# Kernel tuning notes

Measured on AMD Instinct MI355X. Metric: run time of the kernel, lower is better.

Reference implementation:

```python
import jax, jax.numpy as jnp
import numpy as np

NODE_TYPE_SIZE = 9      # common.NodeType.SIZE in MeshGraphNets
N_NODES = 1_000_000
N_CELLS = 2_000_000


def setup_inputs() -> dict:
    key = jax.random.key(0)
    k1, k2, k3, k4, k5 = jax.random.split(key, 5)
    world_pos = jax.random.normal(k1, (1, N_NODES, 3), dtype=jnp.float32)
    prev_world_pos = world_pos + 0.01 * jax.random.normal(k2, (1, N_NODES, 3), dtype=jnp.float32)
    mesh_pos = jax.random.normal(k3, (1, N_NODES, 3), dtype=jnp.float32)
    node_type = jax.random.randint(k4, (1, N_NODES, 1), 0, NODE_TYPE_SIZE, dtype=jnp.int64)
    # random triangles with guaranteed-distinct vertices (avoids degenerate
    # zero-length edges, matching real meshes where triangle corners differ)
    base = jax.random.randint(k5, (N_CELLS, 1), 0, N_NODES, dtype=jnp.int64)
    cells = jnp.mod(base + jnp.arange(3, dtype=jnp.int64)[None, :], N_NODES)[None]
    return {
        'world_pos': world_pos,
        'prev_world_pos': prev_world_pos,
        'mesh_pos': mesh_pos,
        'node_type': node_type,
        'cells': cells,
    }


def _triangles_to_edges(cells):
    # cells: [F, 3] -> bidirectional directed edge list [2 * 3F]
    a, b, c = cells[:, 0], cells[:, 1], cells[:, 2]
    u = jnp.concatenate([a, b, c])  # edge endpoints (a,b),(b,c),(c,a)
    v = jnp.concatenate([b, c, a])
    senders = jnp.concatenate([u, v])
    receivers = jnp.concatenate([v, u])
    return senders, receivers


def reference(world_pos, prev_world_pos, mesh_pos, node_type, cells):
    # squeeze the leading batch dim of 1, as the torch module does
    world_pos = jnp.squeeze(world_pos, 0)          # [N, 3]
    prev_world_pos = jnp.squeeze(prev_world_pos, 0)
    mesh_pos = jnp.squeeze(mesh_pos, 0)
    node_type = jnp.squeeze(node_type, 0)          # [N, 1]
    cells = jnp.squeeze(cells, 0)                  # [F, 3]

    velocity = world_pos - prev_world_pos                                   # [N, 3]
    nt_onehot = jax.nn.one_hot(node_type[:, 0], NODE_TYPE_SIZE,
                               dtype=world_pos.dtype)                        # [N, 9]
    node_features = jnp.concatenate([velocity, nt_onehot], axis=-1)          # [N, 12]

    senders, receivers = _triangles_to_edges(cells)                          # [E]
    rel_world = world_pos[senders] - world_pos[receivers]                    # [E, 3]
    rel_mesh = mesh_pos[senders] - mesh_pos[receivers]                       # [E, 3]
    edge_features = jnp.concatenate([
        rel_world,
        jnp.linalg.norm(rel_world, axis=-1, keepdims=True),
        rel_mesh,
        jnp.linalg.norm(rel_mesh, axis=-1, keepdims=True),
    ], axis=-1)                                                              # [E, 7]
    return node_features, edge_features
```

## Files before the change

kernel.cpp:

```cpp
#include <hip/hip_runtime.h>

typedef float f4 __attribute__((ext_vector_type(4)));

struct F3 { float x, y, z; };
struct I3 { int a, b, c; };

__device__ __forceinline__ F3 ldf3(const float* __restrict__ p) {
    F3 r;
    __builtin_memcpy(&r, p, sizeof(F3));
    return r;
}
__device__ __forceinline__ F3 sub3(F3 a, F3 b) { F3 r{a.x - b.x, a.y - b.y, a.z - b.z}; return r; }
__device__ __forceinline__ float nrm3(F3 v) { return sqrtf(v.x * v.x + v.y * v.y + v.z * v.z); }

__device__ __forceinline__ void putrow(f4* __restrict__ ef, size_t e, size_t er,
                                       F3 rw, F3 rm) {
    float nw = nrm3(rw), nm = nrm3(rm);
    f4 v0 = {rw.x, rw.y, rw.z, nw};
    f4 v1 = {rm.x, rm.y, rm.z, nm};
    f4 v2 = {-rw.x, -rw.y, -rw.z, nw};
    f4 v3 = {-rm.x, -rm.y, -rm.z, nm};
    ef[2 * e + 0]  = v0;
    ef[2 * e + 1]  = v1;
    ef[2 * er + 0] = v2;
    ef[2 * er + 1] = v3;
}

__global__ void __launch_bounds__(256) fused(const float* __restrict__ world,
                                             const float* __restrict__ prev,
                                             const float* __restrict__ mesh,
                                             const int* __restrict__ ntype,
                                             const int* __restrict__ cells,
                                             f4* __restrict__ nf,
                                             f4* __restrict__ ef,
                                             int n_nodes, int n_cells, int edge_blocks) {
    if ((int)blockIdx.x < edge_blocks) {
        int c = blockIdx.x * 256 + threadIdx.x;
        if (c >= n_cells) return;
        I3 t;
        __builtin_memcpy(&t, cells + 3 * (size_t)c, sizeof(I3));

        F3 wa = ldf3(world + 3 * (size_t)t.a);
        F3 wb = ldf3(world + 3 * (size_t)t.b);
        F3 wc = ldf3(world + 3 * (size_t)t.c);
        F3 ma = ldf3(mesh + 3 * (size_t)t.a);
        F3 mb = ldf3(mesh + 3 * (size_t)t.b);
        F3 mc = ldf3(mesh + 3 * (size_t)t.c);

        size_t NC = (size_t)n_cells;
        size_t e = (size_t)c;
        putrow(ef, e,          e + 3 * NC, sub3(wa, wb), sub3(ma, mb));
        putrow(ef, e + NC,     e + 4 * NC, sub3(wb, wc), sub3(mb, mc));
        putrow(ef, e + 2 * NC, e + 5 * NC, sub3(wc, wa), sub3(mc, ma));
    } else {
        int n = (blockIdx.x - edge_blocks) * 256 + threadIdx.x;
        if (n >= n_nodes) return;
        F3 w = ldf3(world + 3 * (size_t)n);
        F3 p = ldf3(prev + 3 * (size_t)n);
        int t = ntype[n];
        f4* dst = nf + 3 * (size_t)n;
        f4 r0 = {w.x - p.x, w.y - p.y, w.z - p.z, t == 0 ? 1.f : 0.f};
        f4 r1 = {t == 1 ? 1.f : 0.f, t == 2 ? 1.f : 0.f, t == 3 ? 1.f : 0.f, t == 4 ? 1.f : 0.f};
        f4 r2 = {t == 5 ? 1.f : 0.f, t == 6 ? 1.f : 0.f, t == 7 ? 1.f : 0.f, t == 8 ? 1.f : 0.f};
        dst[0] = r0;
        dst[1] = r1;
        dst[2] = r2;
    }
}

extern "C" void kernel_launch(void* const* d_in, const int* in_sizes, int n_in,
                              void* d_out, int out_size, void* d_ws, size_t ws_size,
                              hipStream_t stream) {
    const float* world = (const float*)d_in[0];
    const float* prev  = (const float*)d_in[1];
    const float* mesh  = (const float*)d_in[2];
    const int* ntype   = (const int*)d_in[3];
    const int* cells   = (const int*)d_in[4];
    int n_nodes = in_sizes[0] / 3;
    int n_cells = in_sizes[4] / 3;

    float* out = (float*)d_out;
    f4* nf = (f4*)out;
    f4* ef = (f4*)(out + (size_t)n_nodes * 12);

    int edge_blocks = (n_cells + 255) / 256;
    int node_blocks = (n_nodes + 255) / 256;

    fused<<<dim3(edge_blocks + node_blocks), dim3(256), 0, stream>>>(
        world, prev, mesh, ntype, cells, nf, ef, n_nodes, n_cells, edge_blocks);
}
```

Measured before the change: 546.4 us.

## Stage edge and node rows in LDS for coalesced nontemporal stores

Edge and node feature rows are first written to shared memory, then stored to global memory with contiguous per-lane 16-byte nontemporal stores. When a cell's three vertices are consecutive, their coordinates are fetched with one contiguous load instead of three gathers. The aim is better write coalescing, less cache pollution from streaming output, and fewer load instructions. In exchange it adds block-wide barriers and extra LDS traffic, and the fast path only helps meshes with consecutive vertex indices.

```diff
diff --git a/kernel.cpp b/kernel.cpp
--- a/kernel.cpp
+++ b/kernel.cpp
@@ -3,30 +3,21 @@
 typedef float f4 __attribute__((ext_vector_type(4)));
 
 struct F3 { float x, y, z; };
+struct F9 { float v[9]; };
 struct I3 { int a, b, c; };
 
-__device__ __forceinline__ F3 ldf3(const float* __restrict__ p) {
-    F3 r;
-    __builtin_memcpy(&r, p, sizeof(F3));
-    return r;
+#define BLK 256
+
+__device__ __forceinline__ f4 mkf4(float a, float b, float c, float d) {
+    f4 v; v.x = a; v.y = b; v.z = c; v.w = d; return v;
 }
-__device__ __forceinline__ F3 sub3(F3 a, F3 b) { F3 r{a.x - b.x, a.y - b.y, a.z - b.z}; return r; }
+__device__ __forceinline__ F3 sub3p(const float* a, const float* b) {
+    F3 r; r.x = a[0] - b[0]; r.y = a[1] - b[1]; r.z = a[2] - b[2]; return r;
+}
 __device__ __forceinline__ float nrm3(F3 v) { return sqrtf(v.x * v.x + v.y * v.y + v.z * v.z); }
 
-__device__ __forceinline__ void putrow(f4* __restrict__ ef, size_t e, size_t er,
-                                       F3 rw, F3 rm) {
-    float nw = nrm3(rw), nm = nrm3(rm);
-    f4 v0 = {rw.x, rw.y, rw.z, nw};
-    f4 v1 = {rm.x, rm.y, rm.z, nm};
-    f4 v2 = {-rw.x, -rw.y, -rw.z, nw};
-    f4 v3 = {-rm.x, -rm.y, -rm.z, nm};
-    ef[2 * e + 0]  = v0;
-    ef[2 * e + 1]  = v1;
-    ef[2 * er + 0] = v2;
-    ef[2 * er + 1] = v3;
-}
 
-__global__ void __launch_bounds__(256) fused(const float* __restrict__ world,
+__global__ void __launch_bounds__(BLK) fused(const float* __restrict__ world,
                                              const float* __restrict__ prev,
                                              const float* __restrict__ mesh,
                                              const int* __restrict__ ntype,
@@ -34,37 +25,108 @@
                                              f4* __restrict__ nf,
                                              f4* __restrict__ ef,
                                              int n_nodes, int n_cells, int edge_blocks) {
+    __shared__ __align__(16) unsigned char smem[2 * 3 * BLK * 16];
+    int lt = threadIdx.x;
+
     if ((int)blockIdx.x < edge_blocks) {
-        int c = blockIdx.x * 256 + threadIdx.x;
-        if (c >= n_cells) return;
-        I3 t;
-        __builtin_memcpy(&t, cells + 3 * (size_t)c, sizeof(I3));
-
-        F3 wa = ldf3(world + 3 * (size_t)t.a);
-        F3 wb = ldf3(world + 3 * (size_t)t.b);
-        F3 wc = ldf3(world + 3 * (size_t)t.c);
-        F3 ma = ldf3(mesh + 3 * (size_t)t.a);
-        F3 mb = ldf3(mesh + 3 * (size_t)t.b);
-        F3 mc = ldf3(mesh + 3 * (size_t)t.c);
-
+        f4 (*lds)[3][BLK] = (f4 (*)[3][BLK])smem;
+        int c0 = blockIdx.x * BLK;
+        int chunk = min(BLK, n_cells - c0);
+        F3 rw[3], rm[3];
+        float nw[3], nm[3];
+        if (lt < chunk) {
+            I3 t;
+            __builtin_memcpy(&t, cells + 3 * (size_t)(c0 + lt), sizeof(I3));
+            F9 w9, m9;
+            if (t.b == t.a + 1 && t.c == t.a + 2) {
+                __builtin_memcpy(&w9, world + 3 * (size_t)t.a, sizeof(F9));
+                __builtin_memcpy(&m9, mesh  + 3 * (size_t)t.a, sizeof(F9));
+            } else {
+                __builtin_memcpy(&w9.v[0], world + 3 * (size_t)t.a, 12);
+                __builtin_memcpy(&w9.v[3], world + 3 * (size_t)t.b, 12);
+                __builtin_memcpy(&w9.v[6], world + 3 * (size_t)t.c, 12);
+                __builtin_memcpy(&m9.v[0], mesh  + 3 * (size_t)t.a, 12);
+                __builtin_memcpy(&m9.v[3], mesh  + 3 * (size_t)t.b, 12);
+                __builtin_memcpy(&m9.v[6], mesh  + 3 * (size_t)t.c, 12);
+            }
+            rw[0] = sub3p(&w9.v[0], &w9.v[3]); rm[0] = sub3p(&m9.v[0], &m9.v[3]);
+            rw[1] = sub3p(&w9.v[3], &w9.v[6]); rm[1] = sub3p(&m9.v[3], &m9.v[6]);
+            rw[2] = sub3p(&w9.v[6], &w9.v[0]); rm[2] = sub3p(&m9.v[6], &m9.v[0]);
+            #pragma unroll
+            for (int r = 0; r < 3; r++) { nw[r] = nrm3(rw[r]); nm[r] = nrm3(rm[r]); }
+            #pragma unroll
+            for (int r = 0; r < 3; r++) {
+                lds[0][r][lt] = mkf4(rw[r].x, rw[r].y, rw[r].z, nw[r]);
+                lds[1][r][lt] = mkf4(rm[r].x, rm[r].y, rm[r].z, nm[r]);
+            }
+        }
+        __syncthreads();
         size_t NC = (size_t)n_cells;
-        size_t e = (size_t)c;
-        putrow(ef, e,          e + 3 * NC, sub3(wa, wb), sub3(ma, mb));
-        putrow(ef, e + NC,     e + 4 * NC, sub3(wb, wc), sub3(mb, mc));
-        putrow(ef, e + 2 * NC, e + 5 * NC, sub3(wc, wa), sub3(mc, ma));
+        if (chunk == BLK) {
+            #pragma unroll
+            for (int r = 0; r < 3; r++) {
+                f4* G = ef + 2 * ((size_t)r * NC + (size_t)c0);
+                __builtin_nontemporal_store(lds[lt & 1][r][lt >> 1], G + lt);
+                int j = lt + BLK;
+                __builtin_nontemporal_store(lds[j & 1][r][j >> 1], G + j);
+            }
+        } else {
+            for (int r = 0; r < 3; r++) {
+                f4* G = ef + 2 * ((size_t)r * NC + (size_t)c0);
+                for (int j = lt; j < 2 * chunk; j += BLK)
+                    __builtin_nontemporal_store(lds[j & 1][r][j >> 1], G + j);
+            }
+        }
+        __syncthreads();
+        if (lt < chunk) {
+            #pragma unroll
+            for (int r = 0; r < 3; r++) {
+                lds[0][r][lt] = mkf4(-rw[r].x, -rw[r].y, -rw[r].z, nw[r]);
+                lds[1][r][lt] = mkf4(-rm[r].x, -rm[r].y, -rm[r].z, nm[r]);
+            }
+        }
+        __syncthreads();
+        if (chunk == BLK) {
+            #pragma unroll
+            for (int r = 0; r < 3; r++) {
+                f4* G = ef + 2 * (((size_t)r + 3) * NC + (size_t)c0);
+                __builtin_nontemporal_store(lds[lt & 1][r][lt >> 1], G + lt);
+                int j = lt + BLK;
+                __builtin_nontemporal_store(lds[j & 1][r][j >> 1], G + j);
+            }
+        } else {
+            for (int r = 0; r < 3; r++) {
+                f4* G = ef + 2 * (((size_t)r + 3) * NC + (size_t)c0);
+                for (int j = lt; j < 2 * chunk; j += BLK)
+                    __builtin_nontemporal_store(lds[j & 1][r][j >> 1], G + j);
+            }
+        }
     } else {
-        int n = (blockIdx.x - edge_blocks) * 256 + threadIdx.x;
-        if (n >= n_nodes) return;
-        F3 w = ldf3(world + 3 * (size_t)n);
-        F3 p = ldf3(prev + 3 * (size_t)n);
-        int t = ntype[n];
-        f4* dst = nf + 3 * (size_t)n;
-        f4 r0 = {w.x - p.x, w.y - p.y, w.z - p.z, t == 0 ? 1.f : 0.f};
-        f4 r1 = {t == 1 ? 1.f : 0.f, t == 2 ? 1.f : 0.f, t == 3 ? 1.f : 0.f, t == 4 ? 1.f : 0.f};
-        f4 r2 = {t == 5 ? 1.f : 0.f, t == 6 ? 1.f : 0.f, t == 7 ? 1.f : 0.f, t == 8 ? 1.f : 0.f};
-        dst[0] = r0;
-        dst[1] = r1;
-        dst[2] = r2;
+        f4 (*lds)[BLK + 1] = (f4 (*)[BLK + 1])smem;
+        int n0 = (blockIdx.x - edge_blocks) * BLK;
+        int chunk = min(BLK, n_nodes - n0);
+        int n = n0 + lt;
+        if (lt < chunk) {
+            F3 w, p;
+            __builtin_memcpy(&w, world + 3 * (size_t)n, sizeof(F3));
+            __builtin_memcpy(&p, prev + 3 * (size_t)n, sizeof(F3));
+            int t = ntype[n];
+            lds[0][lt] = mkf4(w.x - p.x, w.y - p.y, w.z - p.z, t == 0 ? 1.f : 0.f);
+            lds[1][lt] = mkf4(t == 1 ? 1.f : 0.f, t == 2 ? 1.f : 0.f, t == 3 ? 1.f : 0.f, t == 4 ? 1.f : 0.f);
+            lds[2][lt] = mkf4(t == 5 ? 1.f : 0.f, t == 6 ? 1.f : 0.f, t == 7 ? 1.f : 0.f, t == 8 ? 1.f : 0.f);
+        }
+        __syncthreads();
+        f4* G = nf + 3 * (size_t)n0;
+        if (chunk == BLK) {
+            #pragma unroll
+            for (int m = 0; m < 3; m++) {
+                int j = lt + m * BLK;
+                __builtin_nontemporal_store(lds[j % 3][j / 3], G + j);
+            }
+        } else {
+            for (int j = lt; j < 3 * chunk; j += BLK)
+                __builtin_nontemporal_store(lds[j % 3][j / 3], G + j);
+        }
     }
 }
 
@@ -83,9 +145,9 @@
     f4* nf = (f4*)out;
     f4* ef = (f4*)(out + (size_t)n_nodes * 12);
 
-    int edge_blocks = (n_cells + 255) / 256;
-    int node_blocks = (n_nodes + 255) / 256;
+    int edge_blocks = (n_cells + BLK - 1) / BLK;
+    int node_blocks = (n_nodes + BLK - 1) / BLK;
 
-    fused<<<dim3(edge_blocks + node_blocks), dim3(256), 0, stream>>>(
+    fused<<<dim3(edge_blocks + node_blocks), dim3(BLK), 0, stream>>>(
         world, prev, mesh, ntype, cells, nf, ef, n_nodes, n_cells, edge_blocks);
 }
```

After: 532.9 us. 1.03x faster.
